# Performance work log

Measured on AMD Instinct MI355X. Metric: run time of the kernel, lower is better.

The kernel has to match this reference:

```python
import jax, jax.numpy as jnp
import numpy as np

N, E, M = 8192, 32768, 2048
D, H1, C = 768, 8, 768
NEG_SLOPE = 0.2


def gat_conv(x, src, dst, W, att_src, att_dst, bias, heads, out_ch):
    # PyG GATConv (eval mode, concat=True, add_self_loops already applied to src/dst)
    n = x.shape[0]
    h = (x @ W).reshape(n, heads, out_ch)                      # [N,H,C]
    a_src = jnp.einsum('nhc,hc->nh', h, att_src)               # [N,H]
    a_dst = jnp.einsum('nhc,hc->nh', h, att_dst)
    e = jax.nn.leaky_relu(a_src[src] + a_dst[dst], NEG_SLOPE)  # [E',H]
    # softmax over incoming edges of each dst node
    m = jax.ops.segment_max(e, dst, num_segments=n)
    e = jnp.exp(e - m[dst])
    denom = jax.ops.segment_sum(e, dst, num_segments=n)
    alpha = e / (denom[dst] + 1e-16)                           # [E',H]
    msg = h[src] * alpha[:, :, None]                           # [E',H,C]
    out = jax.ops.segment_sum(msg, dst, num_segments=n)        # [N,H,C]
    return out.reshape(n, heads * out_ch) + bias


def setup_inputs() -> dict:
    key = jax.random.key(0)
    ks = jax.random.split(key, 16)
    s = 0.02
    inp = {
        'x': jax.random.normal(ks[0], (N, D), jnp.float32),
        'edge_index': jax.random.randint(ks[1], (2, E), 0, N, jnp.int64),
        'mask_idx': jax.random.randint(ks[2], (M,), 0, N, jnp.int64),
        'W1': jax.random.normal(ks[3], (D, H1 * C), jnp.float32) * s,
        'att_src1': jax.random.normal(ks[4], (H1, C), jnp.float32) * s,
        'att_dst1': jax.random.normal(ks[5], (H1, C), jnp.float32) * s,
        'b1': jnp.zeros((H1 * C,), jnp.float32),
        'W2': jax.random.normal(ks[6], (H1 * C, C), jnp.float32) * s,
        'att_src2': jax.random.normal(ks[7], (1, C), jnp.float32) * s,
        'att_dst2': jax.random.normal(ks[8], (1, C), jnp.float32) * s,
        'b2': jnp.zeros((C,), jnp.float32),
        # fc: 1536 -> 768, classifier: 768 -> 2
        'fc_w': jax.random.normal(ks[9], (2 * C, C), jnp.float32) * s,
        'fc_b': jnp.zeros((C,), jnp.float32),
        'cls_w': jax.random.normal(ks[10], (C, 2), jnp.float32) * s,
        'cls_b': jnp.zeros((2,), jnp.float32),
    }
    return inp


def reference(x, edge_index, mask_idx, W1, att_src1, att_dst1, b1,
              W2, att_src2, att_dst2, b2, fc_w, fc_b, cls_w, cls_b):
    n = x.shape[0]
    loops = jnp.arange(n, dtype=edge_index.dtype)
    src = jnp.concatenate([edge_index[0], loops])   # PyG default add_self_loops
    dst = jnp.concatenate([edge_index[1], loops])
    h = gat_conv(x, src, dst, W1, att_src1, att_dst1, b1, H1, C)   # [N, 6144]
    h = jax.nn.elu(h)
    h = gat_conv(h, src, dst, W2, att_src2, att_dst2, b2, 1, C)    # [N, 768]
    x_gemb = h[mask_idx]                                           # [M, 768]
    x_emb = x[mask_idx]                                            # [M, 768]
    out = jnp.concatenate([x_gemb, x_emb], axis=1) @ fc_w + fc_b   # [M, 768]
    out = out @ cls_w + cls_b                                      # [M, 2]
    return out
```

## Files before the change

kernel.cpp:

```cpp
#include <hip/hip_runtime.h>

typedef unsigned short ushort_t;
typedef __attribute__((ext_vector_type(8))) __bf16 bf16x8;
typedef __attribute__((ext_vector_type(8))) unsigned short ushort8;
typedef __attribute__((ext_vector_type(4))) unsigned short ushort4v;
typedef __attribute__((ext_vector_type(4))) float f32x4;

#define N_NODES 8192
#define NODE_MASK 8191
#define E_EDGES 32768
#define E_TOT   40960
#define M_MASK  2048
#define D_IN    768
#define C_CH    768
#define F1      6144

typedef __attribute__((address_space(1))) const void* gas_ptr;
typedef __attribute__((address_space(3))) void* las_ptr;

__device__ __forceinline__ float bf2f(ushort_t u) {
    union { unsigned int i; float f; } v; v.i = ((unsigned int)u) << 16; return v.f;
}
__device__ __forceinline__ ushort_t f2bf(float f) {
    union { float f; unsigned int i; } v; v.f = f;
    unsigned int r = v.i + 0x7fffu + ((v.i >> 16) & 1u);
    return (ushort_t)(r >> 16);
}

__global__ void init_kernel(int* deg, int* fill, int* flags) {
    int i = blockIdx.x * 256 + threadIdx.x;
    if (i < N_NODES) { deg[i] = 0; fill[i] = 0; }
    if (i < 2) flags[i] = 0;
}
__global__ void detect_kernel(const int* __restrict__ raw, int nhalf, int* __restrict__ flag) {
    int i = blockIdx.x * 256 + threadIdx.x;
    if (i < nhalf && raw[2 * i + 1] != 0) atomicOr(flag, 1);
}
__global__ void convert_idx_kernel(const void* __restrict__ raw, int n,
                                   const int* __restrict__ flag, int* __restrict__ out) {
    int i = blockIdx.x * 256 + threadIdx.x;
    if (i >= n) return;
    int v = (*flag) ? ((const int*)raw)[i] : (int)((const long long*)raw)[i];
    out[i] = v & NODE_MASK;
}

__global__ void cvt_bf16_kernel(const float* __restrict__ in, ushort_t* __restrict__ out, int n4) {
    int i = blockIdx.x * 256 + threadIdx.x;
    if (i >= n4) return;
    f32x4 v = *(const f32x4*)(in + i * 4);
    ushort_t o0 = f2bf(v[0]), o1 = f2bf(v[1]), o2 = f2bf(v[2]), o3 = f2bf(v[3]);
    unsigned long long pk = (unsigned long long)o0 | ((unsigned long long)o1 << 16)
                          | ((unsigned long long)o2 << 32) | ((unsigned long long)o3 << 48);
    *(unsigned long long*)(out + i * 4) = pk;
}

__global__ __launch_bounds__(256) void transpose_cvt_kernel(
    const float* __restrict__ in, ushort_t* __restrict__ out, int R, int Ccols)
{
    __shared__ ushort_t tile[32][33];
    int tx = threadIdx.x & 31, ty = threadIdx.x >> 5;
    int x  = blockIdx.x * 32 + tx;
    int y0 = blockIdx.y * 32;
#pragma unroll
    for (int i = 0; i < 4; ++i)
        tile[ty + i * 8][tx] = f2bf(in[(size_t)(y0 + ty + i * 8) * Ccols + x]);
    __syncthreads();
#pragma unroll
    for (int i = 0; i < 4; ++i)
        out[(size_t)(blockIdx.x * 32 + ty + i * 8) * R + y0 + tx] = tile[tx][ty + i * 8];
}

__global__ __launch_bounds__(256) void gemm_bt_kernel(
    const ushort_t* __restrict__ A, const ushort_t* __restrict__ Bt,
    ushort_t* __restrict__ C, const float* __restrict__ bias,
    int M, int N, int K)
{
    __shared__ ushort_t lsA[128 * 64];
    __shared__ ushort_t lsB[128 * 64];

    const int tid  = threadIdx.x;
    const int lane = tid & 63;
    const int wave = tid >> 6;
    const int wm = wave >> 1, wn = wave & 1;
    const int bx = blockIdx.x, by = blockIdx.y;

    const f32x4 zero = {0.f, 0.f, 0.f, 0.f};
    f32x4 acc[4][4];
#pragma unroll
    for (int i = 0; i < 4; ++i)
#pragma unroll
        for (int j = 0; j < 4; ++j) acc[i][j] = zero;

    const int l8 = lane >> 3;
    const int c8 = lane & 7;
    const int q  = lane >> 4;
    const int rl = lane & 15;

    for (int kt = 0; kt < K; kt += 64) {
        __syncthreads();
#pragma unroll
        for (int i = 0; i < 4; ++i) {
            int rbase = wave * 32 + i * 8;
            int row   = rbase + l8;
            int gch   = c8 ^ (row & 7);
            const ushort_t* gA = A  + (size_t)(by * 128 + row) * K + kt + gch * 8;
            const ushort_t* gB = Bt + (size_t)(bx * 128 + row) * K + kt + gch * 8;
            __builtin_amdgcn_global_load_lds((gas_ptr)gA, (las_ptr)(lsA + rbase * 64), 16, 0, 0);
            __builtin_amdgcn_global_load_lds((gas_ptr)gB, (las_ptr)(lsB + rbase * 64), 16, 0, 0);
        }
        __syncthreads();
#pragma unroll
        for (int s = 0; s < 2; ++s) {
            bf16x8 af[4], bfv[4];
#pragma unroll
            for (int i = 0; i < 4; ++i) {
                int Ra = wm * 64 + i * 16 + rl;
                af[i]  = *(const bf16x8*)(lsA + Ra * 64 + (((s * 4 + q) ^ (Ra & 7)) * 8));
                int Rb = wn * 64 + i * 16 + rl;
                bfv[i] = *(const bf16x8*)(lsB + Rb * 64 + (((s * 4 + q) ^ (Rb & 7)) * 8));
            }
#pragma unroll
            for (int i = 0; i < 4; ++i)
#pragma unroll
                for (int j = 0; j < 4; ++j)
                    acc[i][j] = __builtin_amdgcn_mfma_f32_16x16x32_bf16(af[i], bfv[j], acc[i][j], 0, 0, 0);
        }
    }
#pragma unroll
    for (int j = 0; j < 4; ++j) {
        int col = bx * 128 + wn * 64 + j * 16 + rl;
        float bv = bias ? bias[col] : 0.0f;
#pragma unroll
        for (int i = 0; i < 4; ++i) {
#pragma unroll
            for (int t = 0; t < 4; ++t) {
                int row = by * 128 + wm * 64 + i * 16 + q * 4 + t;
                C[(size_t)row * N + col] = f2bf(acc[i][j][t] + bv);
            }
        }
    }
}

#define NBX_BD 6
#define NBY_BD 64

__global__ __launch_bounds__(256) void gemm_bd_kernel(
    const ushort_t* __restrict__ A0, const ushort_t* __restrict__ Bt0,
    ushort_t* __restrict__ C, const float* __restrict__ bias,
    int M, int K)
{
    __shared__ ushort_t lsA[128 * 64];
    __shared__ ushort_t lsB[128 * 64];

    const int tid  = threadIdx.x;
    const int lane = tid & 63;
    const int wave = tid >> 6;
    const int wm = wave >> 1, wn = wave & 1;

    const int d    = blockIdx.x;
    const int xcd  = d & 7;
    const int slot = d >> 3;
    const int bx   = slot % NBX_BD;
    const int grp  = xcd * 64 + slot / NBX_BD;
    const int by   = grp & (NBY_BD - 1);
    const int head = grp >> 6;

    const ushort_t* A  = A0  + (size_t)head * M * K;
    const ushort_t* Bt = Bt0 + (size_t)head * C_CH * K;

    const f32x4 zero = {0.f, 0.f, 0.f, 0.f};
    f32x4 acc[4][4];
#pragma unroll
    for (int i = 0; i < 4; ++i)
#pragma unroll
        for (int j = 0; j < 4; ++j) acc[i][j] = zero;

    const int l8 = lane >> 3;
    const int c8 = lane & 7;
    const int q  = lane >> 4;
    const int rl = lane & 15;

    for (int kt = 0; kt < K; kt += 64) {
        __syncthreads();
#pragma unroll
        for (int i = 0; i < 4; ++i) {
            int rbase = wave * 32 + i * 8;
            int row   = rbase + l8;
            int gch   = c8 ^ (row & 7);
            const ushort_t* gA = A  + (size_t)(by * 128 + row) * K + kt + gch * 8;
            const ushort_t* gB = Bt + (size_t)(bx * 128 + row) * K + kt + gch * 8;
            __builtin_amdgcn_global_load_lds((gas_ptr)gA, (las_ptr)(lsA + rbase * 64), 16, 0, 0);
            __builtin_amdgcn_global_load_lds((gas_ptr)gB, (las_ptr)(lsB + rbase * 64), 16, 0, 0);
        }
        __syncthreads();
#pragma unroll
        for (int s = 0; s < 2; ++s) {
            bf16x8 af[4], bfv[4];
#pragma unroll
            for (int i = 0; i < 4; ++i) {
                int Ra = wm * 64 + i * 16 + rl;
                af[i]  = *(const bf16x8*)(lsA + Ra * 64 + (((s * 4 + q) ^ (Ra & 7)) * 8));
                int Rb = wn * 64 + i * 16 + rl;
                bfv[i] = *(const bf16x8*)(lsB + Rb * 64 + (((s * 4 + q) ^ (Rb & 7)) * 8));
            }
#pragma unroll
            for (int i = 0; i < 4; ++i)
#pragma unroll
                for (int j = 0; j < 4; ++j)
                    acc[i][j] = __builtin_amdgcn_mfma_f32_16x16x32_bf16(af[i], bfv[j], acc[i][j], 0, 0, 0);
        }
    }
#pragma unroll
    for (int j = 0; j < 4; ++j) {
        int colf = head * C_CH + bx * 128 + wn * 64 + j * 16 + rl;
        float bv = bias[colf];
#pragma unroll
        for (int i = 0; i < 4; ++i) {
#pragma unroll
            for (int t = 0; t < 4; ++t) {
                int row = by * 128 + wm * 64 + i * 16 + q * 4 + t;
                float v = acc[i][j][t] + bv;
                v = v > 0.f ? v : (__expf(v) - 1.0f);
                C[(size_t)row * F1 + colf] = f2bf(v);
            }
        }
    }
}

#define NBX2 6
#define NBY2 64
#define NSPLIT 2

__global__ __launch_bounds__(256) void gemm_bt_splitk_kernel(
    const ushort_t* __restrict__ A, const ushort_t* __restrict__ Bt,
    float* __restrict__ Cpart, int M, int N, int K)
{
    __shared__ ushort_t lsA[128 * 64];
    __shared__ ushort_t lsB[128 * 64];

    const int tid  = threadIdx.x;
    const int lane = tid & 63;
    const int wave = tid >> 6;
    const int wm = wave >> 1, wn = wave & 1;

    const int d    = blockIdx.x;
    const int xcd  = d & 7;
    const int slot = d >> 3;
    const int bx   = slot % NBX2;
    const int grp  = xcd * 16 + slot / NBX2;
    const int by   = grp & (NBY2 - 1);
    const int bz   = grp >> 6;

    const int kh  = K >> 1;
    const int kt0 = bz * kh;
    float* __restrict__ Cp = Cpart + (size_t)bz * M * N;

    const f32x4 zero = {0.f, 0.f, 0.f, 0.f};
    f32x4 acc[4][4];
#pragma unroll
    for (int i = 0; i < 4; ++i)
#pragma unroll
        for (int j = 0; j < 4; ++j) acc[i][j] = zero;

    const int l8 = lane >> 3;
    const int c8 = lane & 7;
    const int q  = lane >> 4;
    const int rl = lane & 15;

    for (int kt = kt0; kt < kt0 + kh; kt += 64) {
        __syncthreads();
#pragma unroll
        for (int i = 0; i < 4; ++i) {
            int rbase = wave * 32 + i * 8;
            int row   = rbase + l8;
            int gch   = c8 ^ (row & 7);
            const ushort_t* gA = A  + (size_t)(by * 128 + row) * K + kt + gch * 8;
            const ushort_t* gB = Bt + (size_t)(bx * 128 + row) * K + kt + gch * 8;
            __builtin_amdgcn_global_load_lds((gas_ptr)gA, (las_ptr)(lsA + rbase * 64), 16, 0, 0);
            __builtin_amdgcn_global_load_lds((gas_ptr)gB, (las_ptr)(lsB + rbase * 64), 16, 0, 0);
        }
        __syncthreads();
#pragma unroll
        for (int s = 0; s < 2; ++s) {
            bf16x8 af[4], bfv[4];
#pragma unroll
            for (int i = 0; i < 4; ++i) {
                int Ra = wm * 64 + i * 16 + rl;
                af[i]  = *(const bf16x8*)(lsA + Ra * 64 + (((s * 4 + q) ^ (Ra & 7)) * 8));
                int Rb = wn * 64 + i * 16 + rl;
                bfv[i] = *(const bf16x8*)(lsB + Rb * 64 + (((s * 4 + q) ^ (Rb & 7)) * 8));
            }
#pragma unroll
            for (int i = 0; i < 4; ++i)
#pragma unroll
                for (int j = 0; j < 4; ++j)
                    acc[i][j] = __builtin_amdgcn_mfma_f32_16x16x32_bf16(af[i], bfv[j], acc[i][j], 0, 0, 0);
        }
    }
#pragma unroll
    for (int j = 0; j < 4; ++j) {
        int col = bx * 128 + wn * 64 + j * 16 + rl;
#pragma unroll
        for (int i = 0; i < 4; ++i) {
#pragma unroll
            for (int t = 0; t < 4; ++t) {
                int row = by * 128 + wm * 64 + i * 16 + q * 4 + t;
                Cp[(size_t)row * N + col] = acc[i][j][t];
            }
        }
    }
}

__global__ __launch_bounds__(192) void splitk_reduce_att_kernel(
    const float* __restrict__ P0, const float* __restrict__ P1,
    ushort_t* __restrict__ out, const float* __restrict__ as2,
    const float* __restrict__ ad2, float* __restrict__ a_s, float* __restrict__ a_d)
{
    const int n = blockIdx.x, tid = threadIdx.x;
    const int c0 = tid * 4;
    f32x4 a = *(const f32x4*)(P0 + (size_t)n * C_CH + c0);
    f32x4 b = *(const f32x4*)(P1 + (size_t)n * C_CH + c0);
    f32x4 ws = *(const f32x4*)(as2 + c0);
    f32x4 wd = *(const f32x4*)(ad2 + c0);
    float s1 = 0.f, s2 = 0.f;
    ushort_t o[4];
#pragma unroll
    for (int k = 0; k < 4; ++k) {
        float v = a[k] + b[k];
        o[k] = f2bf(v);
        s1 += v * ws[k];
        s2 += v * wd[k];
    }
    unsigned long long pk = (unsigned long long)o[0] | ((unsigned long long)o[1] << 16)
                          | ((unsigned long long)o[2] << 32) | ((unsigned long long)o[3] << 48);
    *(unsigned long long*)(out + (size_t)n * C_CH + c0) = pk;

    __shared__ float red[2][3];
#pragma unroll
    for (int off = 32; off > 0; off >>= 1) {
        s1 += __shfl_down(s1, off);
        s2 += __shfl_down(s2, off);
    }
    const int lane = tid & 63, wv = tid >> 6;
    if (lane == 0) { red[0][wv] = s1; red[1][wv] = s2; }
    __syncthreads();
    if (tid == 0) {
        a_s[n] = red[0][0] + red[0][1] + red[0][2];
        a_d[n] = red[1][0] + red[1][1] + red[1][2];
    }
}

__global__ void indeg_kernel(const int* __restrict__ eic, int* __restrict__ deg) {
    int e = blockIdx.x * 256 + threadIdx.x;
    if (e >= E_TOT) return;
    int dst = (e < E_EDGES) ? eic[E_EDGES + e] : (e - E_EDGES);
    atomicAdd(&deg[dst], 1);
}
__global__ __launch_bounds__(256) void scan_kernel(const int* __restrict__ deg, int* __restrict__ rowptr) {
    __shared__ int part[256];
    int t = threadIdx.x;
    int local[32];
    int s = 0;
#pragma unroll
    for (int i = 0; i < 32; ++i) { local[i] = deg[t * 32 + i]; s += local[i]; }
    part[t] = s;
    __syncthreads();
    for (int off = 1; off < 256; off <<= 1) {
        int v = (t >= off) ? part[t - off] : 0;
        __syncthreads();
        part[t] += v;
        __syncthreads();
    }
    int run = (t == 0) ? 0 : part[t - 1];
#pragma unroll
    for (int i = 0; i < 32; ++i) { rowptr[t * 32 + i] = run; run += local[i]; }
    if (t == 255) rowptr[N_NODES] = run;
}
__global__ void scatter_kernel(const int* __restrict__ eic, const int* __restrict__ rowptr,
                               int* __restrict__ fill, int* __restrict__ csr_src) {
    int e = blockIdx.x * 256 + threadIdx.x;
    if (e >= E_TOT) return;
    int src, dst;
    if (e < E_EDGES) { src = eic[e]; dst = eic[E_EDGES + e]; }
    else             { src = e - E_EDGES; dst = src; }
    int pos = rowptr[dst] + atomicAdd(&fill[dst], 1);
    csr_src[pos] = src;
}

__global__ __launch_bounds__(256) void att1_wprep_kernel(
    const float* __restrict__ W1, const float* __restrict__ att_s,
    const float* __restrict__ att_d, float* __restrict__ ws, float* __restrict__ wd)
{
    int gid  = blockIdx.x * 4 + (threadIdx.x >> 6);
    int lane = threadIdx.x & 63;
    int d = gid >> 3, h = gid & 7;
    const float* wp = W1 + (size_t)d * F1 + h * C_CH;
    const float* sp = att_s + h * C_CH;
    const float* dp = att_d + h * C_CH;
    float s1 = 0.f, s2 = 0.f;
#pragma unroll
    for (int j = 0; j < 3; ++j) {
        int o = j * 256 + lane * 4;
        f32x4 w  = *(const f32x4*)(wp + o);
        f32x4 sv = *(const f32x4*)(sp + o);
        f32x4 dv = *(const f32x4*)(dp + o);
#pragma unroll
        for (int k = 0; k < 4; ++k) { s1 += w[k] * sv[k]; s2 += w[k] * dv[k]; }
    }
#pragma unroll
    for (int off = 32; off > 0; off >>= 1) {
        s1 += __shfl_down(s1, off);
        s2 += __shfl_down(s2, off);
    }
    if (lane == 0) { ws[h * D_IN + d] = s1; wd[h * D_IN + d] = s2; }
}

__global__ __launch_bounds__(256) void att1_gemv_kernel(
    const ushort_t* __restrict__ xb, const float* __restrict__ ws,
    const float* __restrict__ wd, float* __restrict__ a_s, float* __restrict__ a_d)
{
    int n    = blockIdx.x * 4 + (threadIdx.x >> 6);
    int lane = threadIdx.x & 63;
    const ushort_t* xp = xb + (size_t)n * D_IN;
    float s[8], d[8];
#pragma unroll
    for (int h = 0; h < 8; ++h) { s[h] = 0.f; d[h] = 0.f; }
#pragma unroll
    for (int j = 0; j < 3; ++j) {
        int d0 = j * 256 + lane * 4;
        ushort4v xv = *(const ushort4v*)(xp + d0);
        float xf0 = bf2f(xv[0]), xf1 = bf2f(xv[1]), xf2 = bf2f(xv[2]), xf3 = bf2f(xv[3]);
#pragma unroll
        for (int h = 0; h < 8; ++h) {
            f32x4 wv = *(const f32x4*)(ws + (size_t)h * D_IN + d0);
            f32x4 dv = *(const f32x4*)(wd + (size_t)h * D_IN + d0);
            s[h] += xf0 * wv[0] + xf1 * wv[1] + xf2 * wv[2] + xf3 * wv[3];
            d[h] += xf0 * dv[0] + xf1 * dv[1] + xf2 * dv[2] + xf3 * dv[3];
        }
    }
#pragma unroll
    for (int h = 0; h < 8; ++h) {
#pragma unroll
        for (int off = 32; off > 0; off >>= 1) {
            s[h] += __shfl_down(s[h], off);
            d[h] += __shfl_down(d[h], off);
        }
    }
    if (lane == 0) {
#pragma unroll
        for (int h = 0; h < 8; ++h) { a_s[n * 8 + h] = s[h]; a_d[n * 8 + h] = d[h]; }
    }
}

__global__ __launch_bounds__(192) void agg8x_kernel(
    const ushort_t* __restrict__ xb, const float* __restrict__ a_s, const float* __restrict__ a_d,
    const int* __restrict__ rowptr, const int* __restrict__ csr_src,
    ushort_t* __restrict__ xagg)
{
    const int n = blockIdx.x;
    const int tid = threadIdx.x;
    const int base = rowptr[n];
    const int deg  = rowptr[n + 1] - base;

    __shared__ float s_m[8], s_rd[8], s_adst[8];
    __shared__ int   s_src[64];
    __shared__ float s_w[64][8];

    if (tid < 8) {
        float adst = a_d[n * 8 + tid];
        float m = -1e30f;
        for (int e = 0; e < deg; ++e) {
            float scv = a_s[csr_src[base + e] * 8 + tid] + adst;
            scv = scv > 0.f ? scv : 0.2f * scv;
            m = fmaxf(m, scv);
        }
        float den = 0.f;
        for (int e = 0; e < deg; ++e) {
            float scv = a_s[csr_src[base + e] * 8 + tid] + adst;
            scv = scv > 0.f ? scv : 0.2f * scv;
            den += __expf(scv - m);
        }
        s_m[tid] = m; s_rd[tid] = 1.0f / (den + 1e-16f); s_adst[tid] = adst;
    }
    __syncthreads();

    float acc[8][4];
#pragma unroll
    for (int h = 0; h < 8; ++h)
#pragma unroll
        for (int i = 0; i < 4; ++i) acc[h][i] = 0.f;
    const int c0 = tid * 4;

    for (int cs = 0; cs < deg; cs += 64) {
        int cnt = min(64, deg - cs);
        __syncthreads();
        for (int idx = tid; idx < cnt; idx += 192) s_src[idx] = csr_src[base + cs + idx];
        __syncthreads();
        for (int idx = tid; idx < cnt * 8; idx += 192) {
            int e = idx >> 3, hd = idx & 7;
            float scv = a_s[s_src[e] * 8 + hd] + s_adst[hd];
            scv = scv > 0.f ? scv : 0.2f * scv;
            s_w[e][hd] = __expf(scv - s_m[hd]) * s_rd[hd];
        }
        __syncthreads();
        for (int e = 0; e < cnt; ++e) {
            const ushort_t* xp = xb + (size_t)s_src[e] * D_IN + c0;
            ushort4v xv = *(const ushort4v*)(xp);
            float xf0 = bf2f(xv[0]), xf1 = bf2f(xv[1]), xf2 = bf2f(xv[2]), xf3 = bf2f(xv[3]);
#pragma unroll
            for (int h = 0; h < 8; ++h) {
                float w = s_w[e][h];
                acc[h][0] += w * xf0;
                acc[h][1] += w * xf1;
                acc[h][2] += w * xf2;
                acc[h][3] += w * xf3;
            }
        }
    }
#pragma unroll
    for (int h = 0; h < 8; ++h) {
        ushort_t o0 = f2bf(acc[h][0]), o1 = f2bf(acc[h][1]);
        ushort_t o2 = f2bf(acc[h][2]), o3 = f2bf(acc[h][3]);
        unsigned long long pk = (unsigned long long)o0 | ((unsigned long long)o1 << 16)
                              | ((unsigned long long)o2 << 32) | ((unsigned long long)o3 << 48);
        *(unsigned long long*)(xagg + ((size_t)h * N_NODES + n) * D_IN + c0) = pk;
    }
}

__global__ __launch_bounds__(256) void agg1_kernel(
    const ushort_t* __restrict__ h, const float* __restrict__ a_s, const float* __restrict__ a_d,
    const int* __restrict__ rowptr, const int* __restrict__ csr_src,
    const float* __restrict__ bias, ushort_t* __restrict__ out)
{
    const int n    = blockIdx.x * 4 + (threadIdx.x >> 6);
    const int lane = threadIdx.x & 63;
    const int base = rowptr[n];
    const int deg  = rowptr[n + 1] - base;
    const float adst = a_d[n];

    float m = -1e30f;
    for (int cs = 0; cs < deg; cs += 64) {
        int e = cs + lane;
        if (e < deg) {
            float scv = a_s[csr_src[base + e]] + adst;
            scv = scv > 0.f ? scv : 0.2f * scv;
            m = fmaxf(m, scv);
        }
    }
#pragma unroll
    for (int off = 32; off > 0; off >>= 1) m = fmaxf(m, __shfl_xor(m, off));
    float den = 0.f;
    for (int cs = 0; cs < deg; cs += 64) {
        int e = cs + lane;
        if (e < deg) {
            float scv = a_s[csr_src[base + e]] + adst;
            scv = scv > 0.f ? scv : 0.2f * scv;
            den += __expf(scv - m);
        }
    }
#pragma unroll
    for (int off = 32; off > 0; off >>= 1) den += __shfl_xor(den, off);
    const float rd = 1.0f / (den + 1e-16f);

    const int c0 = lane * 12;
    float acc[12];
#pragma unroll
    for (int i = 0; i < 12; ++i) acc[i] = 0.f;

    for (int cs = 0; cs < deg; cs += 64) {
        int cnt = min(64, deg - cs);
        int e = cs + lane;
        int srcl = (e < deg) ? csr_src[base + e] : 0;
        float wv = 0.f;
        if (e < deg) {
            float scv = a_s[srcl] + adst;
            scv = scv > 0.f ? scv : 0.2f * scv;
            wv = __expf(scv - m) * rd;
        }
        for (int k = 0; k < cnt; ++k) {
            int src = __shfl(srcl, k);
            float w = __shfl(wv, k);
            const ushort_t* hp = h + (size_t)src * C_CH + c0;
            ushort4v v0 = *(const ushort4v*)(hp);
            ushort4v v1 = *(const ushort4v*)(hp + 4);
            ushort4v v2 = *(const ushort4v*)(hp + 8);
#pragma unroll
            for (int i = 0; i < 4; ++i) {
                acc[i]     += w * bf2f(v0[i]);
                acc[4 + i] += w * bf2f(v1[i]);
                acc[8 + i] += w * bf2f(v2[i]);
            }
        }
    }
#pragma unroll
    for (int p = 0; p < 3; ++p) {
        ushort_t o0 = f2bf(acc[p * 4 + 0] + bias[c0 + p * 4 + 0]);
        ushort_t o1 = f2bf(acc[p * 4 + 1] + bias[c0 + p * 4 + 1]);
        ushort_t o2 = f2bf(acc[p * 4 + 2] + bias[c0 + p * 4 + 2]);
        ushort_t o3 = f2bf(acc[p * 4 + 3] + bias[c0 + p * 4 + 3]);
        unsigned long long pk = (unsigned long long)o0 | ((unsigned long long)o1 << 16)
                              | ((unsigned long long)o2 << 32) | ((unsigned long long)o3 << 48);
        *(unsigned long long*)(out + (size_t)n * C_CH + c0 + p * 4) = pk;
    }
}

__global__ void gatherfc_kernel(const ushort_t* __restrict__ out2, const ushort_t* __restrict__ xb,
                                const int* __restrict__ maskc, ushort_t* __restrict__ Afc)
{
    int m = blockIdx.x, t = threadIdx.x;
    int mi = maskc[m];
    const ushort_t* p1 = out2 + (size_t)mi * 768;
    const ushort_t* p2 = xb   + (size_t)mi * 768;
    for (int c = t; c < 768; c += 256) {
        Afc[(size_t)m * 1536 + c]       = p1[c];
        Afc[(size_t)m * 1536 + 768 + c] = p2[c];
    }
}

__global__ __launch_bounds__(256) void cls_kernel(
    const ushort_t* __restrict__ fc_out, const float* __restrict__ cls_w,
    const float* __restrict__ cls_b, float* __restrict__ out)
{
    int m = blockIdx.x * 4 + (threadIdx.x >> 6);
    int lane = threadIdx.x & 63;
    float a0 = 0.f, a1 = 0.f;
    const ushort_t* row = fc_out + (size_t)m * 768;
    for (int i = lane; i < 768; i += 64) {
        float v = bf2f(row[i]);
        a0 += v * cls_w[i * 2 + 0];
        a1 += v * cls_w[i * 2 + 1];
    }
#pragma unroll
    for (int off = 32; off > 0; off >>= 1) {
        a0 += __shfl_down(a0, off);
        a1 += __shfl_down(a1, off);
    }
    if (lane == 0) {
        out[m * 2 + 0] = a0 + cls_b[0];
        out[m * 2 + 1] = a1 + cls_b[1];
    }
}

extern "C" void kernel_launch(void* const* d_in, const int* in_sizes, int n_in,
                              void* d_out, int out_size, void* d_ws, size_t ws_size,
                              hipStream_t stream)
{
    const float* x        = (const float*)d_in[0];
    const void*  ei_raw   = d_in[1];
    const void*  mask_raw = d_in[2];
    const float* W1       = (const float*)d_in[3];
    const float* att_src1 = (const float*)d_in[4];
    const float* att_dst1 = (const float*)d_in[5];
    const float* b1       = (const float*)d_in[6];
    const float* W2       = (const float*)d_in[7];
    const float* att_src2 = (const float*)d_in[8];
    const float* att_dst2 = (const float*)d_in[9];
    const float* b2       = (const float*)d_in[10];
    const float* fc_w     = (const float*)d_in[11];
    const float* fc_b     = (const float*)d_in[12];
    const float* cls_w    = (const float*)d_in[13];
    const float* cls_b    = (const float*)d_in[14];
    float* out = (float*)d_out;

    char* ws = (char*)d_ws;
    size_t off = 0;
    auto alloc = [&](size_t bytes) { char* p = ws + off; off = (off + bytes + 255) & ~(size_t)255; return p; };
    int*   flags  = (int*)alloc(2 * 4);
    int*   eic    = (int*)alloc((size_t)2 * E_EDGES * 4);
    int*   maskc  = (int*)alloc((size_t)M_MASK * 4);
    int*   deg    = (int*)alloc(N_NODES * 4);
    int*   fill   = (int*)alloc(N_NODES * 4);
    int*   rowptr = (int*)alloc((N_NODES + 1) * 4);
    int*   csr    = (int*)alloc(E_TOT * 4);
    float* a_s1   = (float*)alloc((size_t)N_NODES * 8 * 4);
    float* a_d1   = (float*)alloc((size_t)N_NODES * 8 * 4);
    float* a_s2   = (float*)alloc((size_t)N_NODES * 4);
    float* a_d2   = (float*)alloc((size_t)N_NODES * 4);
    float* ws1    = (float*)alloc((size_t)D_IN * 8 * 4);
    float* wd1    = (float*)alloc((size_t)D_IN * 8 * 4);
    ushort_t* W1t  = (ushort_t*)alloc((size_t)D_IN * F1 * 2);
    ushort_t* W2t  = (ushort_t*)alloc((size_t)F1 * C_CH * 2);
    ushort_t* fcwt = (ushort_t*)alloc((size_t)1536 * 768 * 2);
    ushort_t* xb   = (ushort_t*)alloc((size_t)N_NODES * D_IN * 2);
    char* region1 = alloc((size_t)N_NODES * F1 * 2);
    char* region2 = alloc((size_t)N_NODES * F1 * 2);
    ushort_t* xagg  = (ushort_t*)region1;
    ushort_t* h2    = (ushort_t*)region1;
    ushort_t* Afc   = (ushort_t*)(region1 + (16u << 20));
    ushort_t* fcout = (ushort_t*)(region1 + (32u << 20));
    float*    part  = (float*)(region1 + (48u << 20));
    ushort_t* out1  = (ushort_t*)region2;
    ushort_t* out2  = (ushort_t*)region2;

    init_kernel<<<N_NODES / 256, 256, 0, stream>>>(deg, fill, flags);
    detect_kernel<<<(E_EDGES + 255) / 256, 256, 0, stream>>>((const int*)ei_raw, E_EDGES, &flags[0]);
    detect_kernel<<<(M_MASK / 2 + 255) / 256, 256, 0, stream>>>((const int*)mask_raw, M_MASK / 2, &flags[1]);
    convert_idx_kernel<<<(2 * E_EDGES + 255) / 256, 256, 0, stream>>>(ei_raw, 2 * E_EDGES, &flags[0], eic);
    convert_idx_kernel<<<(M_MASK + 255) / 256, 256, 0, stream>>>(mask_raw, M_MASK, &flags[1], maskc);
    indeg_kernel<<<E_TOT / 256, 256, 0, stream>>>(eic, deg);
    scan_kernel<<<1, 256, 0, stream>>>(deg, rowptr);
    scatter_kernel<<<E_TOT / 256, 256, 0, stream>>>(eic, rowptr, fill, csr);

    cvt_bf16_kernel<<<(N_NODES * D_IN / 4 + 255) / 256, 256, 0, stream>>>(x, xb, N_NODES * D_IN / 4);
    att1_wprep_kernel<<<(D_IN * 8) / 4, 256, 0, stream>>>(W1, att_src1, att_dst1, ws1, wd1);
    att1_gemv_kernel<<<N_NODES / 4, 256, 0, stream>>>(xb, ws1, wd1, a_s1, a_d1);
    transpose_cvt_kernel<<<dim3(F1 / 32, D_IN / 32), 256, 0, stream>>>(W1, W1t, D_IN, F1);
    transpose_cvt_kernel<<<dim3(C_CH / 32, F1 / 32), 256, 0, stream>>>(W2, W2t, F1, C_CH);
    transpose_cvt_kernel<<<dim3(768 / 32, 1536 / 32), 256, 0, stream>>>(fc_w, fcwt, 1536, 768);

    agg8x_kernel<<<N_NODES, 192, 0, stream>>>(xb, a_s1, a_d1, rowptr, csr, xagg);
    gemm_bd_kernel<<<NBX_BD * NBY_BD * 8, 256, 0, stream>>>(xagg, W1t, out1, b1, N_NODES, D_IN);

    gemm_bt_splitk_kernel<<<NBX2 * NBY2 * NSPLIT, 256, 0, stream>>>(out1, W2t, part, N_NODES, C_CH, F1);
    splitk_reduce_att_kernel<<<N_NODES, 192, 0, stream>>>(
        part, part + (size_t)N_NODES * C_CH, h2, att_src2, att_dst2, a_s2, a_d2);
    agg1_kernel<<<N_NODES / 4, 256, 0, stream>>>(h2, a_s2, a_d2, rowptr, csr, b2, out2);

    gatherfc_kernel<<<M_MASK, 256, 0, stream>>>(out2, xb, maskc, Afc);
    gemm_bt_kernel<<<dim3(768 / 128, M_MASK / 128), 256, 0, stream>>>(Afc, fcwt, fcout, fc_b, M_MASK, 768, 1536);
    cls_kernel<<<M_MASK / 4, 256, 0, stream>>>(fcout, cls_w, cls_b, out);
}
```

Baseline: 469.6 us.

## Use 4-way split-K with bf16 partials and fuse index detect/convert kernels

The second GAT linear GEMM now splits K four ways instead of two, raising the block count from 768 to 1536 so the GPU is better occupied. Partial results are stored as bf16 instead of fp32, which cuts partial-buffer traffic. The reduce kernel sums all four bf16 partials. Separately, the edge and mask index detect/convert kernels are merged into single launches. Rounding each partial to bf16 adds precision loss before the reduction.

New measurement: 826.2 us. +75.9%, slower.

```diff
diff --git a/kernel.cpp b/kernel.cpp
--- a/kernel.cpp
+++ b/kernel.cpp
@@ -32,16 +32,30 @@
     if (i < N_NODES) { deg[i] = 0; fill[i] = 0; }
     if (i < 2) flags[i] = 0;
 }
-__global__ void detect_kernel(const int* __restrict__ raw, int nhalf, int* __restrict__ flag) {
+__global__ void detect2_kernel(const int* __restrict__ raw_e, const int* __restrict__ raw_m,
+                               int* __restrict__ flags) {
     int i = blockIdx.x * 256 + threadIdx.x;
-    if (i < nhalf && raw[2 * i + 1] != 0) atomicOr(flag, 1);
-}
-__global__ void convert_idx_kernel(const void* __restrict__ raw, int n,
-                                   const int* __restrict__ flag, int* __restrict__ out) {
+    if (i < E_EDGES) {
+        if (raw_e[2 * i + 1] != 0) atomicOr(&flags[0], 1);
+    } else {
+        int j = i - E_EDGES;
+        if (j < M_MASK / 2 && raw_m[2 * j + 1] != 0) atomicOr(&flags[1], 1);
+    }
+}
+__global__ void convert2_kernel(const void* __restrict__ ei_raw, const void* __restrict__ mask_raw,
+                                const int* __restrict__ flags,
+                                int* __restrict__ eic, int* __restrict__ maskc) {
     int i = blockIdx.x * 256 + threadIdx.x;
-    if (i >= n) return;
-    int v = (*flag) ? ((const int*)raw)[i] : (int)((const long long*)raw)[i];
-    out[i] = v & NODE_MASK;
+    if (i < 2 * E_EDGES) {
+        int v = flags[0] ? ((const int*)ei_raw)[i] : (int)((const long long*)ei_raw)[i];
+        eic[i] = v & NODE_MASK;
+    } else {
+        int j = i - 2 * E_EDGES;
+        if (j < M_MASK) {
+            int v = flags[1] ? ((const int*)mask_raw)[j] : (int)((const long long*)mask_raw)[j];
+            maskc[j] = v & NODE_MASK;
+        }
+    }
 }
 
 __global__ void cvt_bf16_kernel(const float* __restrict__ in, ushort_t* __restrict__ out, int n4) {
@@ -229,11 +243,11 @@
 
 #define NBX2 6
 #define NBY2 64
-#define NSPLIT 2
+#define NSPLIT 4
 
 __global__ __launch_bounds__(256) void gemm_bt_splitk_kernel(
     const ushort_t* __restrict__ A, const ushort_t* __restrict__ Bt,
-    float* __restrict__ Cpart, int M, int N, int K)
+    ushort_t* __restrict__ Cpart, int M, int N, int K)
 {
     __shared__ ushort_t lsA[128 * 64];
     __shared__ ushort_t lsB[128 * 64];
@@ -247,13 +261,13 @@
     const int xcd  = d & 7;
     const int slot = d >> 3;
     const int bx   = slot % NBX2;
-    const int grp  = xcd * 16 + slot / NBX2;
+    const int grp  = xcd * 32 + slot / NBX2;
     const int by   = grp & (NBY2 - 1);
     const int bz   = grp >> 6;
 
-    const int kh  = K >> 1;
+    const int kh  = K >> 2;
     const int kt0 = bz * kh;
-    float* __restrict__ Cp = Cpart + (size_t)bz * M * N;
+    ushort_t* __restrict__ Cp = Cpart + (size_t)bz * M * N;
 
     const f32x4 zero = {0.f, 0.f, 0.f, 0.f};
     f32x4 acc[4][4];
@@ -305,31 +319,35 @@
 #pragma unroll
             for (int t = 0; t < 4; ++t) {
                 int row = by * 128 + wm * 64 + i * 16 + q * 4 + t;
-                Cp[(size_t)row * N + col] = acc[i][j][t];
+                Cp[(size_t)row * N + col] = f2bf(acc[i][j][t]);
             }
         }
     }
 }
 
 __global__ __launch_bounds__(192) void splitk_reduce_att_kernel(
-    const float* __restrict__ P0, const float* __restrict__ P1,
-    ushort_t* __restrict__ out, const float* __restrict__ as2,
-    const float* __restrict__ ad2, float* __restrict__ a_s, float* __restrict__ a_d)
+    const ushort_t* __restrict__ P, ushort_t* __restrict__ out,
+    const float* __restrict__ as2, const float* __restrict__ ad2,
+    float* __restrict__ a_s, float* __restrict__ a_d)
 {
     const int n = blockIdx.x, tid = threadIdx.x;
     const int c0 = tid * 4;
-    f32x4 a = *(const f32x4*)(P0 + (size_t)n * C_CH + c0);
-    f32x4 b = *(const f32x4*)(P1 + (size_t)n * C_CH + c0);
+    float v[4] = {0.f, 0.f, 0.f, 0.f};
+#pragma unroll
+    for (int k = 0; k < NSPLIT; ++k) {
+        ushort4v p = *(const ushort4v*)(P + ((size_t)k * N_NODES + n) * C_CH + c0);
+#pragma unroll
+        for (int t = 0; t < 4; ++t) v[t] += bf2f(p[t]);
+    }
     f32x4 ws = *(const f32x4*)(as2 + c0);
     f32x4 wd = *(const f32x4*)(ad2 + c0);
     float s1 = 0.f, s2 = 0.f;
     ushort_t o[4];
 #pragma unroll
-    for (int k = 0; k < 4; ++k) {
-        float v = a[k] + b[k];
-        o[k] = f2bf(v);
-        s1 += v * ws[k];
-        s2 += v * wd[k];
+    for (int t = 0; t < 4; ++t) {
+        o[t] = f2bf(v[t]);
+        s1 += v[t] * ws[t];
+        s2 += v[t] * wd[t];
     }
     unsigned long long pk = (unsigned long long)o[0] | ((unsigned long long)o[1] << 16)
                           | ((unsigned long long)o[2] << 32) | ((unsigned long long)o[3] << 48);
@@ -688,15 +706,15 @@
     ushort_t* h2    = (ushort_t*)region1;
     ushort_t* Afc   = (ushort_t*)(region1 + (16u << 20));
     ushort_t* fcout = (ushort_t*)(region1 + (32u << 20));
-    float*    part  = (float*)(region1 + (48u << 20));
+    ushort_t* part  = (ushort_t*)(region1 + (48u << 20));
     ushort_t* out1  = (ushort_t*)region2;
     ushort_t* out2  = (ushort_t*)region2;
 
     init_kernel<<<N_NODES / 256, 256, 0, stream>>>(deg, fill, flags);
-    detect_kernel<<<(E_EDGES + 255) / 256, 256, 0, stream>>>((const int*)ei_raw, E_EDGES, &flags[0]);
-    detect_kernel<<<(M_MASK / 2 + 255) / 256, 256, 0, stream>>>((const int*)mask_raw, M_MASK / 2, &flags[1]);
-    convert_idx_kernel<<<(2 * E_EDGES + 255) / 256, 256, 0, stream>>>(ei_raw, 2 * E_EDGES, &flags[0], eic);
-    convert_idx_kernel<<<(M_MASK + 255) / 256, 256, 0, stream>>>(mask_raw, M_MASK, &flags[1], maskc);
+    detect2_kernel<<<(E_EDGES + M_MASK / 2 + 255) / 256, 256, 0, stream>>>(
+        (const int*)ei_raw, (const int*)mask_raw, flags);
+    convert2_kernel<<<(2 * E_EDGES + M_MASK + 255) / 256, 256, 0, stream>>>(
+        ei_raw, mask_raw, flags, eic, maskc);
     indeg_kernel<<<E_TOT / 256, 256, 0, stream>>>(eic, deg);
     scan_kernel<<<1, 256, 0, stream>>>(deg, rowptr);
     scatter_kernel<<<E_TOT / 256, 256, 0, stream>>>(eic, rowptr, fill, csr);
@@ -713,7 +731,7 @@
 
     gemm_bt_splitk_kernel<<<NBX2 * NBY2 * NSPLIT, 256, 0, stream>>>(out1, W2t, part, N_NODES, C_CH, F1);
     splitk_reduce_att_kernel<<<N_NODES, 192, 0, stream>>>(
-        part, part + (size_t)N_NODES * C_CH, h2, att_src2, att_dst2, a_s2, a_d2);
+        part, h2, att_src2, att_dst2, a_s2, a_d2);
     agg1_kernel<<<N_NODES / 4, 256, 0, stream>>>(h2, a_s2, a_d2, rowptr, csr, b2, out2);
 
     gatherfc_kernel<<<M_MASK, 256, 0, stream>>>(out2, xb, maskc, Afc);
```
